# Kernel optimization log

Hardware: AMD Instinct MI355X
Metric: run time of the kernel (lower is better)

## Reference

```python
import jax, jax.numpy as jnp
import numpy as np

DOWNSAMPLING_K = 64  # number of pooled key/value positions


def setup_inputs() -> dict:
    key = jax.random.key(0)
    ks = jax.random.split(key, 8)
    B, S, H, N, D = 4, 4096, 1024, 16, 64
    s_in = 0.02  # glorot-like scale for H=1024 fan-in
    return {
        "query": jax.random.normal(ks[0], (B, S, H), jnp.float32),
        "key": jax.random.normal(ks[1], (B, S, H), jnp.float32),
        "value": jax.random.normal(ks[2], (B, S, H), jnp.float32),
        "Wq": jax.random.normal(ks[3], (H, N, D), jnp.float32) * s_in,
        "bq": jnp.zeros((N, D), jnp.float32),
        "Wk": jax.random.normal(ks[4], (H, N, D), jnp.float32) * s_in,
        "bk": jnp.zeros((N, D), jnp.float32),
        "Wv": jax.random.normal(ks[5], (H, N, D), jnp.float32) * s_in,
        "bv": jnp.zeros((N, D), jnp.float32),
        "Wo": jax.random.normal(ks[6], (N, D, H), jnp.float32) * s_in,
        "bo": jnp.zeros((H,), jnp.float32),
        "step": 0,
        "train": 0,
    }


def _downsample(x, k):
    # x: [B, S, N, D] -> mean-pool along sequence into k buckets -> [B, k, N, D]
    B, S, N, D = x.shape
    return x.reshape(B, k, S // k, N, D).mean(axis=2)


def reference(query, key, value, Wq, bq, Wk, bk, Wv, bv, Wo, bo, step, train):
    # QKV projections (DenseGeneral features=(num_heads, head_dim))
    q = jnp.einsum("bsh,hnd->bsnd", query, Wq) + bq  # [B,S,N,D]
    k = jnp.einsum("bsh,hnd->bsnd", key, Wk) + bk
    v = jnp.einsum("bsh,hnd->bsnd", value, Wv) + bv
    # Downsampled (sparse) attention: pool K,V to DOWNSAMPLING_K positions
    kd = _downsample(k, DOWNSAMPLING_K)  # [B,K,N,D]
    vd = _downsample(v, DOWNSAMPLING_K)
    scale = 1.0 / jnp.sqrt(jnp.asarray(q.shape[-1], q.dtype))
    scores = jnp.einsum("bsnd,bknd->bnsk", q, kd) * scale  # [B,N,S,K]
    attn = jax.nn.softmax(scores, axis=-1)
    a_v = jnp.einsum("bnsk,bknd->bsnd", attn, vd)  # [B,S,N,D]
    # Output projection (DenseGeneral over (-2,-1))
    out = jnp.einsum("bsnd,ndh->bsh", a_v, Wo) + bo  # [B,S,H]
    return out
```

## Files before the change

kernel.cpp:

```cpp
#include <hip/hip_runtime.h>

typedef unsigned short u16;
typedef unsigned int u32;
typedef __attribute__((ext_vector_type(8))) short bf16x8_t;
typedef __attribute__((ext_vector_type(4))) float f32x4_t;


#define MFMA_BF16 __builtin_amdgcn_mfma_f32_16x16x32_bf16

__device__ __forceinline__ u16 f2bf(float f) {
  union { float f; u32 u; } a; a.f = f;
  u32 u = a.u;
  u32 r = (u + 0x7FFFu + ((u >> 16) & 1u)) >> 16;
  return (u16)r;
}
__device__ __forceinline__ float bf2f(u16 x) {
  union { u32 u; float f; } a; a.u = ((u32)x) << 16; return a.f;
}

__device__ __forceinline__ void async_load16(const void* g, void* l) {
  __builtin_amdgcn_global_load_lds(
      (const __attribute__((address_space(1))) void*)g,
      (__attribute__((address_space(3))) void*)l, 16, 0, 0);
}

__device__ __forceinline__ void stage64(const u16* __restrict__ src,
                                        char* lds_base, int t) {
  const int r = t >> 3;
  const int gch = (t & 7) ^ (r & 7);
  async_load16(src + (size_t)r * 1024 + gch * 8, lds_base + (t >> 6) * 1024);
}

__global__ __launch_bounds__(256) void cvt_bf16(const float* __restrict__ x,
                                                u16* __restrict__ y) {
  const size_t i = (size_t)(blockIdx.x * 256 + threadIdx.x) * 8;
  const float4 a = *(const float4*)(x + i);
  const float4 b = *(const float4*)(x + i + 4);
  bf16x8_t o;
  o[0] = (short)f2bf(a.x); o[1] = (short)f2bf(a.y);
  o[2] = (short)f2bf(a.z); o[3] = (short)f2bf(a.w);
  o[4] = (short)f2bf(b.x); o[5] = (short)f2bf(b.y);
  o[6] = (short)f2bf(b.z); o[7] = (short)f2bf(b.w);
  *(bf16x8_t*)(y + i) = o;
}

__global__ __launch_bounds__(256) void transpose_w4(const float* __restrict__ W0,
                                                    const float* __restrict__ W1,
                                                    const float* __restrict__ W2,
                                                    const float* __restrict__ W3,
                                                    u16* __restrict__ T0, u16* __restrict__ T1,
                                                    u16* __restrict__ T2, u16* __restrict__ T3) {
  const int z = blockIdx.z;
  const float* W = (z == 0) ? W0 : (z == 1) ? W1 : (z == 2) ? W2 : W3;
  u16* WT = (z == 0) ? T0 : (z == 1) ? T1 : (z == 2) ? T2 : T3;
  __shared__ float tile[64][65];
  const int tr = blockIdx.x * 64;
  const int tc = blockIdx.y * 64;
  const int t = threadIdx.x;
#pragma unroll
  for (int i = 0; i < 16; ++i) {
    int idx = i * 256 + t;
    int r = idx >> 6, c = idx & 63;
    tile[r][c] = W[(size_t)(tr + r) * 1024 + tc + c];
  }
  __syncthreads();
#pragma unroll
  for (int i = 0; i < 16; ++i) {
    int idx = i * 256 + t;
    int r = idx >> 6, c = idx & 63;
    WT[(size_t)(tc + r) * 1024 + tr + c] = f2bf(tile[c][r]);
  }
}

__global__ __launch_bounds__(512) void downsample2(const float* __restrict__ key,
                                                   const float* __restrict__ value,
                                                   u16* __restrict__ keyd,
                                                   u16* __restrict__ valued) {
  __shared__ float part[8][256][4];
  const int bkk = blockIdx.x;
  const float* x = blockIdx.y ? value : key;
  u16* xd = blockIdx.y ? valued : keyd;
  const int t = threadIdx.x, lane = t & 63, w = t >> 6;
  const float* base = x + (size_t)bkk * 65536 + (size_t)w * 8 * 1024;
  float4 acc[4] = {{0.f,0.f,0.f,0.f},{0.f,0.f,0.f,0.f},{0.f,0.f,0.f,0.f},{0.f,0.f,0.f,0.f}};
#pragma unroll
  for (int j = 0; j < 8; ++j) {
#pragma unroll
    for (int s = 0; s < 4; ++s) {
      const float4 v = *(const float4*)(base + (size_t)j * 1024 + (s * 64 + lane) * 4);
      acc[s].x += v.x; acc[s].y += v.y; acc[s].z += v.z; acc[s].w += v.w;
    }
  }
#pragma unroll
  for (int s = 0; s < 4; ++s)
    *(float4*)&part[w][s * 64 + lane][0] = acc[s];
  __syncthreads();
  if (t < 256) {
    float4 s = {0.f, 0.f, 0.f, 0.f};
#pragma unroll
    for (int w2 = 0; w2 < 8; ++w2) {
      const float4 v = *(const float4*)&part[w2][t][0];
      s.x += v.x; s.y += v.y; s.z += v.z; s.w += v.w;
    }
    ushort4 r;
    r.x = f2bf(s.x * 0.015625f);
    r.y = f2bf(s.y * 0.015625f);
    r.z = f2bf(s.z * 0.015625f);
    r.w = f2bf(s.w * 0.015625f);
    *(ushort4*)(xd + (size_t)bkk * 1024 + t * 4) = r;
  }
}

__global__ __launch_bounds__(256) void gemm_kv(const u16* __restrict__ A0,
                                               const u16* __restrict__ A1,
                                               const u16* __restrict__ BT0,
                                               const u16* __restrict__ BT1,
                                               const float* __restrict__ bias0,
                                               const float* __restrict__ bias1,
                                               u16* __restrict__ C0,
                                               u16* __restrict__ C1) {
  constexpr int K = 1024, BK = 32;
  __shared__ u16 sA[128 * BK];
  __shared__ u16 sB[128 * BK];
  const int z = blockIdx.z;
  const u16* A = z ? A1 : A0;
  const u16* BT = z ? BT1 : BT0;
  const float* bias = z ? bias1 : bias0;
  u16* Cv = z ? C1 : C0;
  const int t = threadIdx.x;
  const int lane = t & 63;
  const int w = t >> 6;
  const int wr = w >> 1, wc = w & 1;
  const int m0 = blockIdx.x * 128;
  const int n0 = blockIdx.y * 128;
  const int c16 = lane & 15, r16 = lane >> 4;

  f32x4_t acc[4][4] = {};

  for (int k0 = 0; k0 < K; k0 += BK) {
#pragma unroll
    for (int i = 0; i < 2; ++i) {
      const int idx = i * 256 + t;
      const int row = idx >> 2, ch = idx & 3;
      const int gch = ch ^ ((row >> 1) & 3);
      async_load16(A + (size_t)(m0 + row) * K + k0 + gch * 8,
                   (char*)sA + (i * 256 + w * 64) * 16);
    }
#pragma unroll
    for (int i = 0; i < 2; ++i) {
      const int idx = i * 256 + t;
      const int row = idx >> 2, ch = idx & 3;
      const int gch = ch ^ ((row >> 1) & 3);
      async_load16(BT + (size_t)(n0 + row) * K + k0 + gch * 8,
                   (char*)sB + (i * 256 + w * 64) * 16);
    }
    __syncthreads();

    bf16x8_t af[4], bfv[4];
#pragma unroll
    for (int m = 0; m < 4; ++m) {
      const int ra = wr * 64 + m * 16 + c16;
      af[m] = *(const bf16x8_t*)&sA[ra * BK + ((r16 ^ ((ra >> 1) & 3)) << 3)];
    }
#pragma unroll
    for (int n = 0; n < 4; ++n) {
      const int rb = wc * 64 + n * 16 + c16;
      bfv[n] = *(const bf16x8_t*)&sB[rb * BK + ((r16 ^ ((rb >> 1) & 3)) << 3)];
    }
#pragma unroll
    for (int m = 0; m < 4; ++m)
#pragma unroll
      for (int n = 0; n < 4; ++n)
        acc[m][n] = MFMA_BF16(af[m], bfv[n], acc[m][n], 0, 0, 0);
    __syncthreads();
  }

#pragma unroll
  for (int m = 0; m < 4; ++m) {
    const int row0 = m0 + wr * 64 + m * 16 + r16 * 4;
#pragma unroll
    for (int n = 0; n < 4; ++n) {
      const int col = n0 + wc * 64 + n * 16 + c16;
      const float bvl = bias[col];
#pragma unroll
      for (int i = 0; i < 4; ++i) {
        const float val = acc[m][n][i] + bvl;
        if (z)
          Cv[(size_t)col * 256 + row0 + i] = f2bf(val);
        else
          Cv[(size_t)(row0 + i) * 1024 + col] = f2bf(val);
      }
    }
  }
}

template <bool C_BF16>
__global__ __launch_bounds__(512) void gemm256(const u16* __restrict__ A,
                                               const u16* __restrict__ BT,
                                               const float* __restrict__ bias,
                                               void* __restrict__ Cv) {
  __shared__ u16 sAB[65536];
  char* lds = (char*)sAB;
  const int t = threadIdx.x;
  const int lane = t & 63;
  const int w = t >> 6;
  const int wm = w >> 2, wn = w & 3;
  const int c16 = lane & 15, r16 = lane >> 4, c7 = c16 & 7;

  const int tile = (blockIdx.x & 7) * 32 + (blockIdx.x >> 3);
  const int bx = tile >> 2, by = tile & 3;

  const u16* Ab = A + (size_t)bx * 256 * 1024;
  const u16* Bb = BT + (size_t)by * 256 * 1024;

  stage64(Ab,                      lds,                   t);
  stage64(Ab + 128 * 1024,         lds + 128 * 128,       t);
  stage64(Bb,                      lds + 32768,           t);
  stage64(Bb + 64 * 1024,          lds + 32768 + 8192,    t);
  stage64(Bb + 128 * 1024,         lds + 32768 + 16384,   t);
  stage64(Bb + 192 * 1024,         lds + 32768 + 24576,   t);
  stage64(Ab + 64 * 1024,          lds + 64 * 128,        t);
  stage64(Ab + 192 * 1024,         lds + 192 * 128,       t);
  stage64(Ab + 64,                 lds + 65536,           t);
  stage64(Ab + 128 * 1024 + 64,    lds + 65536 + 16384,   t);
  stage64(Bb + 64,                 lds + 98304,           t);
  stage64(Bb + 64 * 1024 + 64,     lds + 98304 + 8192,    t);
  stage64(Bb + 128 * 1024 + 64,    lds + 98304 + 16384,   t);
  stage64(Bb + 192 * 1024 + 64,    lds + 98304 + 24576,   t);
  asm volatile("s_waitcnt vmcnt(6)" ::: "memory");
  __builtin_amdgcn_s_barrier();

  f32x4_t acc[8][4] = {};
  bf16x8_t bf[4][2];

  for (int kt = 0; kt < 16; ++kt) {
    const int slot = kt & 1;
    const u16* sAs = (const u16*)(lds + slot * 65536);
    const u16* sBs = (const u16*)(lds + slot * 65536 + 32768);
    char* sAn = lds + (slot ^ 1) * 65536;
    char* sAc = lds + slot * 65536;
    char* sBc = lds + slot * 65536 + 32768;
    const int k1 = (kt < 15 ? kt + 1 : 15) * 64;
    const int k2 = (kt < 14 ? kt + 2 : 15) * 64;

    bf16x8_t af[4][2];
#pragma unroll
    for (int m = 0; m < 4; ++m) {
      const int row = wm * 128 + m * 16 + c16;
#pragma unroll
      for (int kk = 0; kk < 2; ++kk)
        af[m][kk] = *(const bf16x8_t*)&sAs[row * 64 + (((kk * 4 + r16) ^ c7) << 3)];
    }
#pragma unroll
    for (int n = 0; n < 2; ++n) {
      const int row = wn * 64 + n * 16 + c16;
#pragma unroll
      for (int kk = 0; kk < 2; ++kk)
        bf[n][kk] = *(const bf16x8_t*)&sBs[row * 64 + (((kk * 4 + r16) ^ c7) << 3)];
    }
    stage64(Ab + (size_t)64 * 1024 + k1,  sAn + 64 * 128,  t);
    stage64(Ab + (size_t)192 * 1024 + k1, sAn + 192 * 128, t);
    asm volatile("" ::: "memory");
    __builtin_amdgcn_s_barrier();
    asm volatile("s_waitcnt lgkmcnt(0)" ::: "memory");
    __builtin_amdgcn_sched_barrier(0);
    __builtin_amdgcn_s_setprio(1);
#pragma unroll
    for (int m = 0; m < 4; ++m)
#pragma unroll
      for (int n = 0; n < 2; ++n)
#pragma unroll
        for (int kk = 0; kk < 2; ++kk)
          acc[m][n] = MFMA_BF16(af[m][kk], bf[n][kk], acc[m][n], 0, 0, 0);
    __builtin_amdgcn_s_setprio(0);
    asm volatile("" ::: "memory");
    __builtin_amdgcn_s_barrier();
#pragma unroll
    for (int n = 2; n < 4; ++n) {
      const int row = wn * 64 + n * 16 + c16;
#pragma unroll
      for (int kk = 0; kk < 2; ++kk)
        bf[n][kk] = *(const bf16x8_t*)&sBs[row * 64 + (((kk * 4 + r16) ^ c7) << 3)];
    }
    stage64(Ab + k2,                      sAc,             t);
    stage64(Ab + (size_t)128 * 1024 + k2, sAc + 128 * 128, t);
    asm volatile("" ::: "memory");
    __builtin_amdgcn_s_barrier();
    asm volatile("s_waitcnt lgkmcnt(0)" ::: "memory");
    __builtin_amdgcn_sched_barrier(0);
    __builtin_amdgcn_s_setprio(1);
#pragma unroll
    for (int m = 0; m < 4; ++m)
#pragma unroll
      for (int n = 2; n < 4; ++n)
#pragma unroll
        for (int kk = 0; kk < 2; ++kk)
          acc[m][n] = MFMA_BF16(af[m][kk], bf[n][kk], acc[m][n], 0, 0, 0);
    __builtin_amdgcn_s_setprio(0);
    asm volatile("s_waitcnt vmcnt(10)" ::: "memory");
    __builtin_amdgcn_s_barrier();
#pragma unroll
    for (int m = 0; m < 4; ++m) {
      const int row = wm * 128 + 64 + m * 16 + c16;
#pragma unroll
      for (int kk = 0; kk < 2; ++kk)
        af[m][kk] = *(const bf16x8_t*)&sAs[row * 64 + (((kk * 4 + r16) ^ c7) << 3)];
    }
    stage64(Bb + k2,                     sBc,           t);
    stage64(Bb + (size_t)64 * 1024 + k2, sBc + 8192,    t);
    asm volatile("" ::: "memory");
    __builtin_amdgcn_s_barrier();
    asm volatile("s_waitcnt lgkmcnt(0)" ::: "memory");
    __builtin_amdgcn_sched_barrier(0);
    __builtin_amdgcn_s_setprio(1);
#pragma unroll
    for (int m = 0; m < 4; ++m)
#pragma unroll
      for (int n = 0; n < 2; ++n)
#pragma unroll
        for (int kk = 0; kk < 2; ++kk)
          acc[4 + m][n] = MFMA_BF16(af[m][kk], bf[n][kk], acc[4 + m][n], 0, 0, 0);
    __builtin_amdgcn_s_setprio(0);
    asm volatile("" ::: "memory");
    __builtin_amdgcn_s_barrier();
    stage64(Bb + (size_t)128 * 1024 + k2, sBc + 16384, t);
    stage64(Bb + (size_t)192 * 1024 + k2, sBc + 24576, t);
    asm volatile("" ::: "memory");
    __builtin_amdgcn_s_barrier();
    __builtin_amdgcn_sched_barrier(0);
    __builtin_amdgcn_s_setprio(1);
#pragma unroll
    for (int m = 0; m < 4; ++m)
#pragma unroll
      for (int n = 2; n < 4; ++n)
#pragma unroll
        for (int kk = 0; kk < 2; ++kk)
          acc[4 + m][n] = MFMA_BF16(af[m][kk], bf[n][kk], acc[4 + m][n], 0, 0, 0);
    __builtin_amdgcn_s_setprio(0);
    asm volatile("s_waitcnt vmcnt(8)" ::: "memory");
    __builtin_amdgcn_s_barrier();
  }

#pragma unroll
  for (int m = 0; m < 8; ++m) {
    const int grow = bx * 256 + wm * 128 + m * 16 + r16 * 4;
#pragma unroll
    for (int n = 0; n < 4; ++n) {
      const int col = by * 256 + wn * 64 + n * 16 + c16;
      const float bvl = bias[col];
#pragma unroll
      for (int i = 0; i < 4; ++i) {
        const float val = acc[m][n][i] + bvl;
        if constexpr (C_BF16)
          ((u16*)Cv)[(size_t)(grow + i) * 1024 + col] = f2bf(val);
        else
          ((float*)Cv)[(size_t)(grow + i) * 1024 + col] = val;
      }
    }
  }
}

__global__ __launch_bounds__(256) void attn_mfma(const u16* __restrict__ qb,
                                                 const u16* __restrict__ kdb,
                                                 const u16* __restrict__ vdTb,
                                                 u16* __restrict__ av) {
  __shared__ u16 sKD[64 * 64];
  __shared__ u16 sVD[64 * 64];
  __shared__ u16 sP[4][16 * 64];
  const int t = threadIdx.x;
  const int lane = t & 63;
  const int w = t >> 6;
  const int c16 = lane & 15;
  const int g = lane >> 4;
  const int stile = blockIdx.x, n = blockIdx.y, b = blockIdx.z;
  const int srow_base = b * 4096 + stile * 256 + w * 64;

  bf16x8_t aq[4][2];
#pragma unroll
  for (int st = 0; st < 4; ++st)
#pragma unroll
    for (int dt = 0; dt < 2; ++dt)
      aq[st][dt] = *(const bf16x8_t*)(qb + (size_t)(srow_base + st * 16 + c16) * 1024 +
                                      n * 64 + dt * 32 + g * 8);

#pragma unroll
  for (int c = 0; c < 2; ++c) {
    const int kk = c * 32 + (t >> 3);
    const int colb = ((t & 7) ^ (kk & 7)) << 4;
    async_load16((const char*)kdb + (size_t)(b * 64 + kk) * 2048 + n * 128 + colb,
                 (char*)sKD + c * 4096 + w * 1024);
  }
#pragma unroll
  for (int c = 0; c < 2; ++c) {
    const int dd = c * 32 + (t >> 3);
    const int colb = ((t & 7) ^ (dd & 7)) << 4;
    async_load16((const char*)vdTb + (size_t)(n * 64 + dd) * 512 + b * 128 + colb,
                 (char*)sVD + c * 4096 + w * 1024);
  }
  __syncthreads();

  const int swz = (c16 & 7) << 4;

  for (int st = 0; st < 4; ++st) {
    f32x4_t accs[4];
#pragma unroll
    for (int nn = 0; nn < 4; ++nn) {
      const u16* kr = &sKD[(nn * 16 + c16) * 64];
      bf16x8_t b0 = *(const bf16x8_t*)&kr[((g * 16) ^ swz) >> 1];
      bf16x8_t b1 = *(const bf16x8_t*)&kr[((64 + g * 16) ^ swz) >> 1];
      f32x4_t a = {0.f, 0.f, 0.f, 0.f};
      a = MFMA_BF16(aq[st][0], b0, a, 0, 0, 0);
      a = MFMA_BF16(aq[st][1], b1, a, 0, 0, 0);
      accs[nn] = a;
    }
    float ex[4][4], rs[4];
#pragma unroll
    for (int i = 0; i < 4; ++i) {
      float m = fmaxf(fmaxf(accs[0][i], accs[1][i]), fmaxf(accs[2][i], accs[3][i]));
#pragma unroll
      for (int off = 1; off < 16; off <<= 1) m = fmaxf(m, __shfl_xor(m, off));
      m *= 0.125f;
      float s = 0.f;
#pragma unroll
      for (int nn = 0; nn < 4; ++nn) {
        float e = __expf(accs[nn][i] * 0.125f - m);
        ex[nn][i] = e;
        s += e;
      }
#pragma unroll
      for (int off = 1; off < 16; off <<= 1) s += __shfl_xor(s, off);
      rs[i] = 1.f / s;
    }
#pragma unroll
    for (int i = 0; i < 4; ++i) {
      const int row = g * 4 + i;
      const int rsw = (row & 7) << 4;
#pragma unroll
      for (int nn = 0; nn < 4; ++nn)
        sP[w][row * 64 + (((nn * 32 + c16 * 2) ^ rsw) >> 1)] = f2bf(ex[nn][i]);
    }
    bf16x8_t pa0 = *(const bf16x8_t*)&sP[w][c16 * 64 + (((g * 16) ^ swz) >> 1)];
    bf16x8_t pa1 = *(const bf16x8_t*)&sP[w][c16 * 64 + (((64 + g * 16) ^ swz) >> 1)];
    f32x4_t accv[4];
#pragma unroll
    for (int dt = 0; dt < 4; ++dt) {
      const u16* vr = &sVD[(dt * 16 + c16) * 64];
      bf16x8_t v0 = *(const bf16x8_t*)&vr[((g * 16) ^ swz) >> 1];
      bf16x8_t v1 = *(const bf16x8_t*)&vr[((64 + g * 16) ^ swz) >> 1];
      f32x4_t a = {0.f, 0.f, 0.f, 0.f};
      a = MFMA_BF16(pa0, v0, a, 0, 0, 0);
      a = MFMA_BF16(pa1, v1, a, 0, 0, 0);
      accv[dt] = a;
    }
#pragma unroll
    for (int i = 0; i < 4; ++i) {
      const int row = g * 4 + i;
      const int rsw = (row & 7) << 4;
#pragma unroll
      for (int dt = 0; dt < 4; ++dt)
        sP[w][row * 64 + (((dt * 32 + c16 * 2) ^ rsw) >> 1)] = f2bf(accv[dt][i] * rs[i]);
    }
#pragma unroll
    for (int r = 0; r < 2; ++r) {
      const int row = r * 8 + (lane >> 3);
      const int cb = ((lane & 7) * 16) ^ ((row & 7) << 4);
      bf16x8_t vv = *(const bf16x8_t*)&sP[w][row * 64 + (cb >> 1)];
      *(bf16x8_t*)(av + (size_t)(srow_base + st * 16 + row) * 1024 + n * 64 + (lane & 7) * 8) = vv;
    }
  }
}

extern "C" void kernel_launch(void* const* d_in, const int* in_sizes, int n_in,
                              void* d_out, int out_size, void* d_ws, size_t ws_size,
                              hipStream_t stream) {
  (void)in_sizes; (void)n_in; (void)out_size; (void)ws_size;
  const float* query = (const float*)d_in[0];
  const float* key   = (const float*)d_in[1];
  const float* value = (const float*)d_in[2];
  const float* Wq = (const float*)d_in[3];
  const float* bq = (const float*)d_in[4];
  const float* Wk = (const float*)d_in[5];
  const float* bk = (const float*)d_in[6];
  const float* Wv = (const float*)d_in[7];
  const float* bv = (const float*)d_in[8];
  const float* Wo = (const float*)d_in[9];
  const float* bo = (const float*)d_in[10];
  float* out = (float*)d_out;

  char* ws = (char*)d_ws;
  const size_t MB = 1024 * 1024;
  u16* WqT    = (u16*)(ws + 0 * MB);
  u16* WkT    = (u16*)(ws + 2 * MB);
  u16* WvT    = (u16*)(ws + 4 * MB);
  u16* WoT    = (u16*)(ws + 6 * MB);
  u16* keyd   = (u16*)(ws + 8 * MB);
  u16* valued = (u16*)(ws + 8 * MB + 512 * 1024);
  u16* kdb    = (u16*)(ws + 9 * MB);
  u16* vdTb   = (u16*)(ws + 9 * MB + 512 * 1024);
  u16* avb    = (u16*)(ws + 10 * MB);
  u16* qbuf   = (u16*)d_out;
  u16* qcvt   = (u16*)((char*)d_out + 32 * MB);

  dim3 blk(256);

  cvt_bf16<<<8192, blk, 0, stream>>>(query, qcvt);
  transpose_w4<<<dim3(16, 16, 4), blk, 0, stream>>>(Wq, Wk, Wv, Wo, WqT, WkT, WvT, WoT);
  downsample2<<<dim3(256, 2), 512, 0, stream>>>(key, value, keyd, valued);

  gemm_kv<<<dim3(2, 8, 2), blk, 0, stream>>>(keyd, valued, WkT, WvT, bk, bv, kdb, vdTb);

  gemm256<true><<<256, 512, 0, stream>>>(qcvt, WqT, bq, qbuf);
  attn_mfma<<<dim3(16, 16, 4), blk, 0, stream>>>(qbuf, kdb, vdTb, avb);
  gemm256<false><<<256, 512, 0, stream>>>(avb, WoT, bo, out);
}
```

Baseline: 171.7 us.

## Fuse Q projection GEMM with downsampled attention into one kernel

The Q-projection GEMM main loop moves into a macro and is reused by a new kernel that runs the attention step directly in its epilogue. Each 256x256 tile covers four heads over 256 rows. The Q values go to LDS as bf16, the pooled K/V for those heads are loaded into the spare LDS slot, and each wave does softmax attention for its head. This removes the Q round-trip through global memory and one kernel launch. In exchange the epilogue gets longer and more serialized, and the attention work is spread over only 256 blocks.

```diff
diff --git a/kernel.cpp b/kernel.cpp
--- a/kernel.cpp
+++ b/kernel.cpp
@@ -194,6 +194,112 @@
   }
 }
 
+#define GEMM256_KLOOP(A_, BT_)                                                          \
+  const u16* Ab = (A_) + (size_t)bx * 256 * 1024;                                       \
+  const u16* Bb = (BT_) + (size_t)by * 256 * 1024;                                      \
+  stage64(Ab,                   lds,                 t);                                \
+  stage64(Ab + 128 * 1024,      lds + 128 * 128,     t);                                \
+  stage64(Bb,                   lds + 32768,         t);                                \
+  stage64(Bb + 64 * 1024,       lds + 32768 + 8192,  t);                                \
+  stage64(Bb + 128 * 1024,      lds + 32768 + 16384, t);                                \
+  stage64(Bb + 192 * 1024,      lds + 32768 + 24576, t);                                \
+  stage64(Ab + 64 * 1024,       lds + 64 * 128,      t);                                \
+  stage64(Ab + 192 * 1024,      lds + 192 * 128,     t);                                \
+  stage64(Ab + 64,              lds + 65536,         t);                                \
+  stage64(Ab + 128 * 1024 + 64, lds + 65536 + 16384, t);                                \
+  stage64(Bb + 64,              lds + 98304,         t);                                \
+  stage64(Bb + 64 * 1024 + 64,  lds + 98304 + 8192,  t);                                \
+  stage64(Bb + 128 * 1024 + 64, lds + 98304 + 16384, t);                                \
+  stage64(Bb + 192 * 1024 + 64, lds + 98304 + 24576, t);                                \
+  asm volatile("s_waitcnt vmcnt(6)" ::: "memory");                                      \
+  __builtin_amdgcn_s_barrier();                                                         \
+  for (int kt = 0; kt < 16; ++kt) {                                                     \
+    const int slot = kt & 1;                                                            \
+    const u16* sAs = (const u16*)(lds + slot * 65536);                                  \
+    const u16* sBs = (const u16*)(lds + slot * 65536 + 32768);                          \
+    char* sAn = lds + (slot ^ 1) * 65536;                                               \
+    char* sAc = lds + slot * 65536;                                                     \
+    char* sBc = lds + slot * 65536 + 32768;                                             \
+    const int k1 = (kt < 15 ? kt + 1 : 15) * 64;                                        \
+    const int k2 = (kt < 14 ? kt + 2 : 15) * 64;                                        \
+    bf16x8_t af[4][2];                                                                  \
+    _Pragma("unroll") for (int m = 0; m < 4; ++m) {                                     \
+      const int row = wm * 128 + m * 16 + c16;                                          \
+      _Pragma("unroll") for (int kk = 0; kk < 2; ++kk)                                  \
+        af[m][kk] = *(const bf16x8_t*)&sAs[row * 64 + (((kk * 4 + r16) ^ c7) << 3)];    \
+    }                                                                                   \
+    _Pragma("unroll") for (int n = 0; n < 2; ++n) {                                     \
+      const int row = wn * 64 + n * 16 + c16;                                           \
+      _Pragma("unroll") for (int kk = 0; kk < 2; ++kk)                                  \
+        bfr[n][kk] = *(const bf16x8_t*)&sBs[row * 64 + (((kk * 4 + r16) ^ c7) << 3)];   \
+    }                                                                                   \
+    stage64(Ab + (size_t)64 * 1024 + k1,  sAn + 64 * 128,  t);                          \
+    stage64(Ab + (size_t)192 * 1024 + k1, sAn + 192 * 128, t);                          \
+    asm volatile("" ::: "memory");                                                      \
+    __builtin_amdgcn_s_barrier();                                                       \
+    asm volatile("s_waitcnt lgkmcnt(0)" ::: "memory");                                  \
+    __builtin_amdgcn_sched_barrier(0);                                                  \
+    __builtin_amdgcn_s_setprio(1);                                                      \
+    _Pragma("unroll") for (int m = 0; m < 4; ++m)                                       \
+      _Pragma("unroll") for (int n = 0; n < 2; ++n)                                     \
+        _Pragma("unroll") for (int kk = 0; kk < 2; ++kk)                                \
+          acc[m][n] = MFMA_BF16(af[m][kk], bfr[n][kk], acc[m][n], 0, 0, 0);             \
+    __builtin_amdgcn_s_setprio(0);                                                      \
+    asm volatile("" ::: "memory");                                                      \
+    __builtin_amdgcn_s_barrier();                                                       \
+    _Pragma("unroll") for (int n = 2; n < 4; ++n) {                                     \
+      const int row = wn * 64 + n * 16 + c16;                                           \
+      _Pragma("unroll") for (int kk = 0; kk < 2; ++kk)                                  \
+        bfr[n][kk] = *(const bf16x8_t*)&sBs[row * 64 + (((kk * 4 + r16) ^ c7) << 3)];   \
+    }                                                                                   \
+    stage64(Ab + k2,                      sAc,             t);                          \
+    stage64(Ab + (size_t)128 * 1024 + k2, sAc + 128 * 128, t);                          \
+    asm volatile("" ::: "memory");                                                      \
+    __builtin_amdgcn_s_barrier();                                                       \
+    asm volatile("s_waitcnt lgkmcnt(0)" ::: "memory");                                  \
+    __builtin_amdgcn_sched_barrier(0);                                                  \
+    __builtin_amdgcn_s_setprio(1);                                                      \
+    _Pragma("unroll") for (int m = 0; m < 4; ++m)                                       \
+      _Pragma("unroll") for (int n = 2; n < 4; ++n)                                     \
+        _Pragma("unroll") for (int kk = 0; kk < 2; ++kk)                                \
+          acc[m][n] = MFMA_BF16(af[m][kk], bfr[n][kk], acc[m][n], 0, 0, 0);             \
+    __builtin_amdgcn_s_setprio(0);                                                      \
+    asm volatile("s_waitcnt vmcnt(10)" ::: "memory");                                   \
+    __builtin_amdgcn_s_barrier();                                                       \
+    _Pragma("unroll") for (int m = 0; m < 4; ++m) {                                     \
+      const int row = wm * 128 + 64 + m * 16 + c16;                                     \
+      _Pragma("unroll") for (int kk = 0; kk < 2; ++kk)                                  \
+        af[m][kk] = *(const bf16x8_t*)&sAs[row * 64 + (((kk * 4 + r16) ^ c7) << 3)];    \
+    }                                                                                   \
+    stage64(Bb + k2,                     sBc,        t);                                \
+    stage64(Bb + (size_t)64 * 1024 + k2, sBc + 8192, t);                                \
+    asm volatile("" ::: "memory");                                                      \
+    __builtin_amdgcn_s_barrier();                                                       \
+    asm volatile("s_waitcnt lgkmcnt(0)" ::: "memory");                                  \
+    __builtin_amdgcn_sched_barrier(0);                                                  \
+    __builtin_amdgcn_s_setprio(1);                                                      \
+    _Pragma("unroll") for (int m = 0; m < 4; ++m)                                       \
+      _Pragma("unroll") for (int n = 0; n < 2; ++n)                                     \
+        _Pragma("unroll") for (int kk = 0; kk < 2; ++kk)                                \
+          acc[4 + m][n] = MFMA_BF16(af[m][kk], bfr[n][kk], acc[4 + m][n], 0, 0, 0);     \
+    __builtin_amdgcn_s_setprio(0);                                                      \
+    asm volatile("" ::: "memory");                                                      \
+    __builtin_amdgcn_s_barrier();                                                       \
+    stage64(Bb + (size_t)128 * 1024 + k2, sBc + 16384, t);                              \
+    stage64(Bb + (size_t)192 * 1024 + k2, sBc + 24576, t);                              \
+    asm volatile("" ::: "memory");                                                      \
+    __builtin_amdgcn_s_barrier();                                                       \
+    __builtin_amdgcn_sched_barrier(0);                                                  \
+    __builtin_amdgcn_s_setprio(1);                                                      \
+    _Pragma("unroll") for (int m = 0; m < 4; ++m)                                       \
+      _Pragma("unroll") for (int n = 2; n < 4; ++n)                                     \
+        _Pragma("unroll") for (int kk = 0; kk < 2; ++kk)                                \
+          acc[4 + m][n] = MFMA_BF16(af[m][kk], bfr[n][kk], acc[4 + m][n], 0, 0, 0);     \
+    __builtin_amdgcn_s_setprio(0);                                                      \
+    asm volatile("s_waitcnt vmcnt(8)" ::: "memory");                                    \
+    __builtin_amdgcn_s_barrier();                                                       \
+  }
+
 template <bool C_BF16>
 __global__ __launch_bounds__(512) void gemm256(const u16* __restrict__ A,
                                                const u16* __restrict__ BT,
@@ -206,141 +312,11 @@
   const int w = t >> 6;
   const int wm = w >> 2, wn = w & 3;
   const int c16 = lane & 15, r16 = lane >> 4, c7 = c16 & 7;
-
   const int tile = (blockIdx.x & 7) * 32 + (blockIdx.x >> 3);
   const int bx = tile >> 2, by = tile & 3;
-
-  const u16* Ab = A + (size_t)bx * 256 * 1024;
-  const u16* Bb = BT + (size_t)by * 256 * 1024;
-
-  stage64(Ab,                      lds,                   t);
-  stage64(Ab + 128 * 1024,         lds + 128 * 128,       t);
-  stage64(Bb,                      lds + 32768,           t);
-  stage64(Bb + 64 * 1024,          lds + 32768 + 8192,    t);
-  stage64(Bb + 128 * 1024,         lds + 32768 + 16384,   t);
-  stage64(Bb + 192 * 1024,         lds + 32768 + 24576,   t);
-  stage64(Ab + 64 * 1024,          lds + 64 * 128,        t);
-  stage64(Ab + 192 * 1024,         lds + 192 * 128,       t);
-  stage64(Ab + 64,                 lds + 65536,           t);
-  stage64(Ab + 128 * 1024 + 64,    lds + 65536 + 16384,   t);
-  stage64(Bb + 64,                 lds + 98304,           t);
-  stage64(Bb + 64 * 1024 + 64,     lds + 98304 + 8192,    t);
-  stage64(Bb + 128 * 1024 + 64,    lds + 98304 + 16384,   t);
-  stage64(Bb + 192 * 1024 + 64,    lds + 98304 + 24576,   t);
-  asm volatile("s_waitcnt vmcnt(6)" ::: "memory");
-  __builtin_amdgcn_s_barrier();
-
   f32x4_t acc[8][4] = {};
-  bf16x8_t bf[4][2];
-
-  for (int kt = 0; kt < 16; ++kt) {
-    const int slot = kt & 1;
-    const u16* sAs = (const u16*)(lds + slot * 65536);
-    const u16* sBs = (const u16*)(lds + slot * 65536 + 32768);
-    char* sAn = lds + (slot ^ 1) * 65536;
-    char* sAc = lds + slot * 65536;
-    char* sBc = lds + slot * 65536 + 32768;
-    const int k1 = (kt < 15 ? kt + 1 : 15) * 64;
-    const int k2 = (kt < 14 ? kt + 2 : 15) * 64;
-
-    bf16x8_t af[4][2];
-#pragma unroll
-    for (int m = 0; m < 4; ++m) {
-      const int row = wm * 128 + m * 16 + c16;
-#pragma unroll
-      for (int kk = 0; kk < 2; ++kk)
-        af[m][kk] = *(const bf16x8_t*)&sAs[row * 64 + (((kk * 4 + r16) ^ c7) << 3)];
-    }
-#pragma unroll
-    for (int n = 0; n < 2; ++n) {
-      const int row = wn * 64 + n * 16 + c16;
-#pragma unroll
-      for (int kk = 0; kk < 2; ++kk)
-        bf[n][kk] = *(const bf16x8_t*)&sBs[row * 64 + (((kk * 4 + r16) ^ c7) << 3)];
-    }
-    stage64(Ab + (size_t)64 * 1024 + k1,  sAn + 64 * 128,  t);
-    stage64(Ab + (size_t)192 * 1024 + k1, sAn + 192 * 128, t);
-    asm volatile("" ::: "memory");
-    __builtin_amdgcn_s_barrier();
-    asm volatile("s_waitcnt lgkmcnt(0)" ::: "memory");
-    __builtin_amdgcn_sched_barrier(0);
-    __builtin_amdgcn_s_setprio(1);
-#pragma unroll
-    for (int m = 0; m < 4; ++m)
-#pragma unroll
-      for (int n = 0; n < 2; ++n)
-#pragma unroll
-        for (int kk = 0; kk < 2; ++kk)
-          acc[m][n] = MFMA_BF16(af[m][kk], bf[n][kk], acc[m][n], 0, 0, 0);
-    __builtin_amdgcn_s_setprio(0);
-    asm volatile("" ::: "memory");
-    __builtin_amdgcn_s_barrier();
-#pragma unroll
-    for (int n = 2; n < 4; ++n) {
-      const int row = wn * 64 + n * 16 + c16;
-#pragma unroll
-      for (int kk = 0; kk < 2; ++kk)
-        bf[n][kk] = *(const bf16x8_t*)&sBs[row * 64 + (((kk * 4 + r16) ^ c7) << 3)];
-    }
-    stage64(Ab + k2,                      sAc,             t);
-    stage64(Ab + (size_t)128 * 1024 + k2, sAc + 128 * 128, t);
-    asm volatile("" ::: "memory");
-    __builtin_amdgcn_s_barrier();
-    asm volatile("s_waitcnt lgkmcnt(0)" ::: "memory");
-    __builtin_amdgcn_sched_barrier(0);
-    __builtin_amdgcn_s_setprio(1);
-#pragma unroll
-    for (int m = 0; m < 4; ++m)
-#pragma unroll
-      for (int n = 2; n < 4; ++n)
-#pragma unroll
-        for (int kk = 0; kk < 2; ++kk)
-          acc[m][n] = MFMA_BF16(af[m][kk], bf[n][kk], acc[m][n], 0, 0, 0);
-    __builtin_amdgcn_s_setprio(0);
-    asm volatile("s_waitcnt vmcnt(10)" ::: "memory");
-    __builtin_amdgcn_s_barrier();
-#pragma unroll
-    for (int m = 0; m < 4; ++m) {
-      const int row = wm * 128 + 64 + m * 16 + c16;
-#pragma unroll
-      for (int kk = 0; kk < 2; ++kk)
-        af[m][kk] = *(const bf16x8_t*)&sAs[row * 64 + (((kk * 4 + r16) ^ c7) << 3)];
-    }
-    stage64(Bb + k2,                     sBc,           t);
-    stage64(Bb + (size_t)64 * 1024 + k2, sBc + 8192,    t);
-    asm volatile("" ::: "memory");
-    __builtin_amdgcn_s_barrier();
-    asm volatile("s_waitcnt lgkmcnt(0)" ::: "memory");
-    __builtin_amdgcn_sched_barrier(0);
-    __builtin_amdgcn_s_setprio(1);
-#pragma unroll
-    for (int m = 0; m < 4; ++m)
-#pragma unroll
-      for (int n = 0; n < 2; ++n)
-#pragma unroll
-        for (int kk = 0; kk < 2; ++kk)
-          acc[4 + m][n] = MFMA_BF16(af[m][kk], bf[n][kk], acc[4 + m][n], 0, 0, 0);
-    __builtin_amdgcn_s_setprio(0);
-    asm volatile("" ::: "memory");
-    __builtin_amdgcn_s_barrier();
-    stage64(Bb + (size_t)128 * 1024 + k2, sBc + 16384, t);
-    stage64(Bb + (size_t)192 * 1024 + k2, sBc + 24576, t);
-    asm volatile("" ::: "memory");
-    __builtin_amdgcn_s_barrier();
-    __builtin_amdgcn_sched_barrier(0);
-    __builtin_amdgcn_s_setprio(1);
-#pragma unroll
-    for (int m = 0; m < 4; ++m)
-#pragma unroll
-      for (int n = 2; n < 4; ++n)
-#pragma unroll
-        for (int kk = 0; kk < 2; ++kk)
-          acc[4 + m][n] = MFMA_BF16(af[m][kk], bf[n][kk], acc[4 + m][n], 0, 0, 0);
-    __builtin_amdgcn_s_setprio(0);
-    asm volatile("s_waitcnt vmcnt(8)" ::: "memory");
-    __builtin_amdgcn_s_barrier();
-  }
-
+  bf16x8_t bfr[4][2];
+  GEMM256_KLOOP(A, BT)
 #pragma unroll
   for (int m = 0; m < 8; ++m) {
     const int grow = bx * 256 + wm * 128 + m * 16 + r16 * 4;
@@ -360,112 +336,153 @@
   }
 }
 
-__global__ __launch_bounds__(256) void attn_mfma(const u16* __restrict__ qb,
-                                                 const u16* __restrict__ kdb,
-                                                 const u16* __restrict__ vdTb,
-                                                 u16* __restrict__ av) {
-  __shared__ u16 sKD[64 * 64];
-  __shared__ u16 sVD[64 * 64];
-  __shared__ u16 sP[4][16 * 64];
+__global__ __launch_bounds__(512) void gemm256_attn(const u16* __restrict__ A,
+                                                    const u16* __restrict__ BT,
+                                                    const float* __restrict__ bias,
+                                                    const u16* __restrict__ kdb,
+                                                    const u16* __restrict__ vdTb,
+                                                    u16* __restrict__ av) {
+  __shared__ u16 sAB[65536];
+  char* lds = (char*)sAB;
   const int t = threadIdx.x;
   const int lane = t & 63;
   const int w = t >> 6;
-  const int c16 = lane & 15;
-  const int g = lane >> 4;
-  const int stile = blockIdx.x, n = blockIdx.y, b = blockIdx.z;
-  const int srow_base = b * 4096 + stile * 256 + w * 64;
-
-  bf16x8_t aq[4][2];
-#pragma unroll
-  for (int st = 0; st < 4; ++st)
-#pragma unroll
-    for (int dt = 0; dt < 2; ++dt)
-      aq[st][dt] = *(const bf16x8_t*)(qb + (size_t)(srow_base + st * 16 + c16) * 1024 +
-                                      n * 64 + dt * 32 + g * 8);
-
-#pragma unroll
-  for (int c = 0; c < 2; ++c) {
-    const int kk = c * 32 + (t >> 3);
+  const int wm = w >> 2, wn = w & 3;
+  const int c16 = lane & 15, r16 = lane >> 4, c7 = c16 & 7;
+  const int tile = (blockIdx.x & 7) * 32 + (blockIdx.x >> 3);
+  const int bx = tile >> 2, by = tile & 3;
+  f32x4_t acc[8][4] = {};
+  bf16x8_t bfr[4][2];
+  GEMM256_KLOOP(A, BT)
+
+  asm volatile("s_waitcnt vmcnt(0)" ::: "memory");
+  __builtin_amdgcn_s_barrier();
+
+  const int b = bx >> 4;
+  const int s0b = (bx & 15) * 256;
+  char* kdL = lds + 65536;
+  char* vdL = lds + 65536 + 32768;
+  {
+    const int kk = t >> 3;
     const int colb = ((t & 7) ^ (kk & 7)) << 4;
-    async_load16((const char*)kdb + (size_t)(b * 64 + kk) * 2048 + n * 128 + colb,
-                 (char*)sKD + c * 4096 + w * 1024);
-  }
-#pragma unroll
-  for (int c = 0; c < 2; ++c) {
-    const int dd = c * 32 + (t >> 3);
-    const int colb = ((t & 7) ^ (dd & 7)) << 4;
-    async_load16((const char*)vdTb + (size_t)(n * 64 + dd) * 512 + b * 128 + colb,
-                 (char*)sVD + c * 4096 + w * 1024);
-  }
-  __syncthreads();
-
+#pragma unroll
+    for (int h = 0; h < 4; ++h) {
+      const int n = by * 4 + h;
+      async_load16((const char*)kdb + (size_t)(b * 64 + kk) * 2048 + n * 128 + colb,
+                   kdL + h * 8192 + (t >> 6) * 1024);
+      async_load16((const char*)vdTb + (size_t)(n * 64 + kk) * 512 + b * 128 + colb,
+                   vdL + h * 8192 + (t >> 6) * 1024);
+    }
+  }
+  u16* qh = (u16*)(lds + w * 8192);
+  const int n_head = by * 4 + wn;
+  const u16* kdw = (const u16*)(kdL + wn * 8192);
+  const u16* vdw = (const u16*)(vdL + wn * 8192);
   const int swz = (c16 & 7) << 4;
 
-  for (int st = 0; st < 4; ++st) {
-    f32x4_t accs[4];
-#pragma unroll
-    for (int nn = 0; nn < 4; ++nn) {
-      const u16* kr = &sKD[(nn * 16 + c16) * 64];
-      bf16x8_t b0 = *(const bf16x8_t*)&kr[((g * 16) ^ swz) >> 1];
-      bf16x8_t b1 = *(const bf16x8_t*)&kr[((64 + g * 16) ^ swz) >> 1];
-      f32x4_t a = {0.f, 0.f, 0.f, 0.f};
-      a = MFMA_BF16(aq[st][0], b0, a, 0, 0, 0);
-      a = MFMA_BF16(aq[st][1], b1, a, 0, 0, 0);
-      accs[nn] = a;
-    }
-    float ex[4][4], rs[4];
-#pragma unroll
-    for (int i = 0; i < 4; ++i) {
-      float m = fmaxf(fmaxf(accs[0][i], accs[1][i]), fmaxf(accs[2][i], accs[3][i]));
-#pragma unroll
-      for (int off = 1; off < 16; off <<= 1) m = fmaxf(m, __shfl_xor(m, off));
-      m *= 0.125f;
-      float s = 0.f;
+  for (int half = 0; half < 2; ++half) {
+    asm volatile("s_waitcnt lgkmcnt(0)" ::: "memory");
+#pragma unroll
+    for (int m = 0; m < 4; ++m)
+#pragma unroll
+      for (int nq = 0; nq < 4; ++nq) {
+        const int d = nq * 16 + c16;
+        const float bvl = bias[n_head * 64 + d];
+#pragma unroll
+        for (int i = 0; i < 4; ++i) {
+          const int row = m * 16 + r16 * 4 + i;
+          qh[(row * 128 + ((d * 2) ^ ((row & 7) << 4))) >> 1] =
+              f2bf(acc[half * 4 + m][nq][i] + bvl);
+        }
+      }
+    if (half == 0) {
+      asm volatile("s_waitcnt vmcnt(0) lgkmcnt(0)" ::: "memory");
+      __builtin_amdgcn_s_barrier();
+    } else {
+      asm volatile("s_waitcnt lgkmcnt(0)" ::: "memory");
+    }
+    bf16x8_t aq[4][2];
+#pragma unroll
+    for (int st = 0; st < 4; ++st) {
+      const int row = st * 16 + c16;
+      const int rsw = (row & 7) << 4;
+#pragma unroll
+      for (int dt = 0; dt < 2; ++dt)
+        aq[st][dt] = *(const bf16x8_t*)&qh[(row * 128 + ((dt * 64 + r16 * 16) ^ rsw)) >> 1];
+    }
+    asm volatile("s_waitcnt lgkmcnt(0)" ::: "memory");
+    __builtin_amdgcn_sched_barrier(0);
+    u16* sP = qh;
+
+    for (int st = 0; st < 4; ++st) {
+      f32x4_t accs[4];
 #pragma unroll
       for (int nn = 0; nn < 4; ++nn) {
-        float e = __expf(accs[nn][i] * 0.125f - m);
-        ex[nn][i] = e;
-        s += e;
-      }
-#pragma unroll
-      for (int off = 1; off < 16; off <<= 1) s += __shfl_xor(s, off);
-      rs[i] = 1.f / s;
-    }
-#pragma unroll
-    for (int i = 0; i < 4; ++i) {
-      const int row = g * 4 + i;
-      const int rsw = (row & 7) << 4;
-#pragma unroll
-      for (int nn = 0; nn < 4; ++nn)
-        sP[w][row * 64 + (((nn * 32 + c16 * 2) ^ rsw) >> 1)] = f2bf(ex[nn][i]);
-    }
-    bf16x8_t pa0 = *(const bf16x8_t*)&sP[w][c16 * 64 + (((g * 16) ^ swz) >> 1)];
-    bf16x8_t pa1 = *(const bf16x8_t*)&sP[w][c16 * 64 + (((64 + g * 16) ^ swz) >> 1)];
-    f32x4_t accv[4];
-#pragma unroll
-    for (int dt = 0; dt < 4; ++dt) {
-      const u16* vr = &sVD[(dt * 16 + c16) * 64];
-      bf16x8_t v0 = *(const bf16x8_t*)&vr[((g * 16) ^ swz) >> 1];
-      bf16x8_t v1 = *(const bf16x8_t*)&vr[((64 + g * 16) ^ swz) >> 1];
-      f32x4_t a = {0.f, 0.f, 0.f, 0.f};
-      a = MFMA_BF16(pa0, v0, a, 0, 0, 0);
-      a = MFMA_BF16(pa1, v1, a, 0, 0, 0);
-      accv[dt] = a;
-    }
-#pragma unroll
-    for (int i = 0; i < 4; ++i) {
-      const int row = g * 4 + i;
-      const int rsw = (row & 7) << 4;
-#pragma unroll
-      for (int dt = 0; dt < 4; ++dt)
-        sP[w][row * 64 + (((dt * 32 + c16 * 2) ^ rsw) >> 1)] = f2bf(accv[dt][i] * rs[i]);
-    }
-#pragma unroll
-    for (int r = 0; r < 2; ++r) {
-      const int row = r * 8 + (lane >> 3);
-      const int cb = ((lane & 7) * 16) ^ ((row & 7) << 4);
-      bf16x8_t vv = *(const bf16x8_t*)&sP[w][row * 64 + (cb >> 1)];
-      *(bf16x8_t*)(av + (size_t)(srow_base + st * 16 + row) * 1024 + n * 64 + (lane & 7) * 8) = vv;
+        const u16* kr = &kdw[(nn * 16 + c16) * 64];
+        bf16x8_t b0 = *(const bf16x8_t*)&kr[((r16 * 16) ^ swz) >> 1];
+        bf16x8_t b1 = *(const bf16x8_t*)&kr[((64 + r16 * 16) ^ swz) >> 1];
+        f32x4_t a = {0.f, 0.f, 0.f, 0.f};
+        a = MFMA_BF16(aq[st][0], b0, a, 0, 0, 0);
+        a = MFMA_BF16(aq[st][1], b1, a, 0, 0, 0);
+        accs[nn] = a;
+      }
+      float ex[4][4], rs[4];
+#pragma unroll
+      for (int i = 0; i < 4; ++i) {
+        float m = fmaxf(fmaxf(accs[0][i], accs[1][i]), fmaxf(accs[2][i], accs[3][i]));
+#pragma unroll
+        for (int off = 1; off < 16; off <<= 1) m = fmaxf(m, __shfl_xor(m, off));
+        m *= 0.125f;
+        float s = 0.f;
+#pragma unroll
+        for (int nn = 0; nn < 4; ++nn) {
+          float e = __expf(accs[nn][i] * 0.125f - m);
+          ex[nn][i] = e;
+          s += e;
+        }
+#pragma unroll
+        for (int off = 1; off < 16; off <<= 1) s += __shfl_xor(s, off);
+        rs[i] = 1.f / s;
+      }
+#pragma unroll
+      for (int i = 0; i < 4; ++i) {
+        const int row = r16 * 4 + i;
+        const int rsw = (row & 7) << 4;
+#pragma unroll
+        for (int nn = 0; nn < 4; ++nn)
+          sP[row * 64 + (((nn * 32 + c16 * 2) ^ rsw) >> 1)] = f2bf(ex[nn][i]);
+      }
+      asm volatile("s_waitcnt lgkmcnt(0)" ::: "memory");
+      bf16x8_t pa0 = *(const bf16x8_t*)&sP[c16 * 64 + (((r16 * 16) ^ swz) >> 1)];
+      bf16x8_t pa1 = *(const bf16x8_t*)&sP[c16 * 64 + (((64 + r16 * 16) ^ swz) >> 1)];
+      f32x4_t accv[4];
+#pragma unroll
+      for (int dt = 0; dt < 4; ++dt) {
+        const u16* vr = &vdw[(dt * 16 + c16) * 64];
+        bf16x8_t v0 = *(const bf16x8_t*)&vr[((r16 * 16) ^ swz) >> 1];
+        bf16x8_t v1 = *(const bf16x8_t*)&vr[((64 + r16 * 16) ^ swz) >> 1];
+        f32x4_t a = {0.f, 0.f, 0.f, 0.f};
+        a = MFMA_BF16(pa0, v0, a, 0, 0, 0);
+        a = MFMA_BF16(pa1, v1, a, 0, 0, 0);
+        accv[dt] = a;
+      }
+#pragma unroll
+      for (int i = 0; i < 4; ++i) {
+        const int row = r16 * 4 + i;
+        const int rsw = (row & 7) << 4;
+#pragma unroll
+        for (int dt = 0; dt < 4; ++dt)
+          sP[row * 64 + (((dt * 32 + c16 * 2) ^ rsw) >> 1)] = f2bf(accv[dt][i] * rs[i]);
+      }
+      asm volatile("s_waitcnt lgkmcnt(0)" ::: "memory");
+      const int srow_base = b * 4096 + s0b + wm * 128 + half * 64 + st * 16;
+#pragma unroll
+      for (int r = 0; r < 2; ++r) {
+        const int row = r * 8 + (lane >> 3);
+        const int cb = ((lane & 7) * 16) ^ ((row & 7) << 4);
+        bf16x8_t vv = *(const bf16x8_t*)&sP[row * 64 + (cb >> 1)];
+        *(bf16x8_t*)(av + (size_t)(srow_base + row) * 1024 + n_head * 64 + (lane & 7) * 8) = vv;
+      }
     }
   }
 }
@@ -498,7 +515,6 @@
   u16* kdb    = (u16*)(ws + 9 * MB);
   u16* vdTb   = (u16*)(ws + 9 * MB + 512 * 1024);
   u16* avb    = (u16*)(ws + 10 * MB);
-  u16* qbuf   = (u16*)d_out;
   u16* qcvt   = (u16*)((char*)d_out + 32 * MB);
 
   dim3 blk(256);
@@ -509,7 +525,6 @@
 
   gemm_kv<<<dim3(2, 8, 2), blk, 0, stream>>>(keyd, valued, WkT, WvT, bk, bv, kdb, vdTb);
 
-  gemm256<true><<<256, 512, 0, stream>>>(qcvt, WqT, bq, qbuf);
-  attn_mfma<<<dim3(16, 16, 4), blk, 0, stream>>>(qbuf, kdb, vdTb, avb);
+  gemm256_attn<<<256, 512, 0, stream>>>(qcvt, WqT, bq, kdb, vdTb, avb);
   gemm256<false><<<256, 512, 0, stream>>>(avb, WoT, bo, out);
 }
```

New measurement: 224.4 us. 30.7% more time.
